# Kernel optimization log

Hardware: AMD Instinct MI355X
Metric: run time of the kernel (lower is better)

The kernel has to match this reference:

```python
import jax, jax.numpy as jnp
import numpy as np

BS = 512          # graphs in batch
G = 5             # n_freq_bands
EL = 32           # electrodes per graph
IN = 5            # in_channels
HC = 64           # first_hc == hidden_channels
N = BS * G * EL   # 81920 nodes
E = N * 16        # 1310720 edges
NC = 3            # n_classes
NUM_LAYERS = 2


def setup_inputs() -> dict:
    key = jax.random.key(0)
    ks = jax.random.split(key, 16)
    s = 0.05
    return {
        "x": jax.random.normal(ks[0], (N, IN), jnp.float32),
        "edge_index": jax.random.randint(ks[1], (2, E), 0, N, dtype=jnp.int32),
        "edge_attr": jax.random.uniform(ks[2], (E,), jnp.float32),
        # GatedGraphConv propagation weights: [num_layers, HC, HC]
        "Wg": jax.random.normal(ks[3], (NUM_LAYERS, HC, HC), jnp.float32) * s,
        # GRUCell params (torch layout: gates r,z,n stacked)
        "w_ih": jax.random.normal(ks[4], (3 * HC, HC), jnp.float32) * s,
        "w_hh": jax.random.normal(ks[5], (3 * HC, HC), jnp.float32) * s,
        "b_ih": jnp.zeros((3 * HC,), jnp.float32),
        "b_hh": jnp.zeros((3 * HC,), jnp.float32),
        # MLP head (torch Linear layout: [out, in])
        "W1": jax.random.normal(ks[6], (HC, G * EL * HC), jnp.float32) * s,
        "b1": jnp.zeros((HC,), jnp.float32),
        "W2": jax.random.normal(ks[7], (HC // 2, HC), jnp.float32) * s,
        "b2": jnp.zeros((HC // 2,), jnp.float32),
        "W3": jax.random.normal(ks[8], (HC // 4, HC // 2), jnp.float32) * s,
        "b3": jnp.zeros((HC // 4,), jnp.float32),
        "W4": jax.random.normal(ks[9], (NC, HC // 4), jnp.float32) * s,
        "b4": jnp.zeros((NC,), jnp.float32),
    }


def _gru_cell(m, h, w_ih, w_hh, b_ih, b_hh):
    gi = m @ w_ih.T + b_ih
    gh = h @ w_hh.T + b_hh
    i_r, i_z, i_n = jnp.split(gi, 3, axis=-1)
    h_r, h_z, h_n = jnp.split(gh, 3, axis=-1)
    r = jax.nn.sigmoid(i_r + h_r)
    z = jax.nn.sigmoid(i_z + h_z)
    n = jnp.tanh(i_n + r * h_n)
    return (1.0 - z) * n + z * h


def reference(x, edge_index, edge_attr, Wg, w_ih, w_hh, b_ih, b_hh,
              W1, b1, W2, b2, W3, b3, W4, b4):
    # GatedGraphConv: zero-pad input features to HC
    h = jnp.pad(x, ((0, 0), (0, HC - IN)))  # [N, HC]
    src, dst = edge_index[0], edge_index[1]
    for i in range(NUM_LAYERS):
        m = h @ Wg[i]                               # [N, HC]
        msg = m[src] * edge_attr[:, None]           # [E, HC] gather + weight
        aggr = jax.ops.segment_sum(msg, dst, num_segments=N)  # scatter-add
        h = _gru_cell(aggr, h, w_ih, w_hh, b_ih, b_hh)
    # rearrange '(bs g e) f -> bs (e g f)'
    h = h.reshape(BS, G, EL, HC).transpose(0, 2, 1, 3).reshape(BS, EL * G * HC)
    z = jax.nn.relu(h @ W1.T + b1)
    z = jax.nn.relu(z @ W2.T + b2)
    z = jax.nn.relu(z @ W3.T + b3)
    logits = z @ W4.T + b4
    return jax.nn.softmax(logits, axis=-1)
```

## Files before the change

kernel.cpp:

```cpp
#include <hip/hip_runtime.h>
#include <cstdint>

#define BSZ 512
#define NG 5
#define NEL 32
#define IN_C 5
#define HC 64
#define NN (BSZ * NG * NEL)
#define NE (NN * 16)
#define NC 3
#define KTOT (NG * NEL * HC)
#define NSLICE 16
#define NCB 160
#define CCHUNK (NE / NCB)
#define SORTCAP 9728

typedef __attribute__((ext_vector_type(8))) short bf16x8;
typedef __attribute__((ext_vector_type(4))) float f32x4;

__device__ __forceinline__ float bcast(float v, int l) {
  return __int_as_float(__builtin_amdgcn_readlane(__float_as_int(v), l));
}

__device__ __forceinline__ ushort bf16r(float f) {
  unsigned u = __float_as_uint(f);
  return (ushort)((u + 0x7FFFu + ((u >> 16) & 1u)) >> 16);
}

__device__ __forceinline__ float bf16f(ushort s) {
  return __uint_as_float(((unsigned)s) << 16);
}

__device__ __forceinline__ bf16x8 packf4(float4 x, float4 y) {
  bf16x8 r;
  r[0] = (short)bf16r(x.x); r[1] = (short)bf16r(x.y);
  r[2] = (short)bf16r(x.z); r[3] = (short)bf16r(x.w);
  r[4] = (short)bf16r(y.x); r[5] = (short)bf16r(y.y);
  r[6] = (short)bf16r(y.z); r[7] = (short)bf16r(y.w);
  return r;
}

__device__ __forceinline__ float sigmoidf_(float x) {
  return 1.0f / (1.0f + __expf(-x));
}

__device__ __forceinline__ float tanhf_(float x) {
  x = fminf(fmaxf(x, -15.0f), 15.0f);
  float e = __expf(2.0f * x);
  return (e - 1.0f) / (e + 1.0f);
}

__global__ void k_init(const float* __restrict__ x, float* __restrict__ h) {
  int idx = blockIdx.x * 256 + threadIdx.x;
  int n = idx >> 6, c = idx & 63;
  h[idx] = (c < IN_C) ? x[n * IN_C + c] : 0.0f;
}

__global__ void __launch_bounds__(256) k_chist(const int* __restrict__ ei,
                                               int* __restrict__ ghist) {
  __shared__ int lh[NCB];
  const int t = threadIdx.x;
  if (t < NCB) lh[t] = 0;
  __syncthreads();
  const int base = blockIdx.x * CCHUNK;
  for (int k = t; k < CCHUNK; k += 256)
    atomicAdd(&lh[ei[NE + base + k] >> 9], 1);
  __syncthreads();
  if (t < NCB) ghist[t * NCB + blockIdx.x] = lh[t];
}

__global__ void k_cscan(const int* __restrict__ ghist, int* __restrict__ cstart,
                        int* __restrict__ gof) {
  __shared__ int tot[NCB];
  __shared__ int cs[NCB + 1];
  const int t = threadIdx.x;
  if (t < NCB) {
    int s = 0;
    const int* g = ghist + t * NCB;
    for (int blk = 0; blk < NCB; ++blk) s += g[blk];
    tot[t] = s;
  }
  __syncthreads();
  if (t == 0) {
    int run = 0;
    for (int i = 0; i < NCB; ++i) { cs[i] = run; run += tot[i]; }
    cs[NCB] = run;
  }
  __syncthreads();
  if (t < NCB + 1) cstart[t] = cs[t];
  if (t < NCB) {
    int run = cs[t];
    const int* g = ghist + t * NCB;
    int* go = gof + t * NCB;
    for (int blk = 0; blk < NCB; ++blk) { go[blk] = run; run += g[blk]; }
  }
}

__global__ void __launch_bounds__(256) k_cpart(const int* __restrict__ ei,
                                               const float* __restrict__ ea,
                                               const int* __restrict__ gof,
                                               int* __restrict__ ent4,
                                               ushort* __restrict__ dstlo) {
  __shared__ int cur[NCB];
  const int t = threadIdx.x;
  if (t < NCB) cur[t] = gof[t * NCB + blockIdx.x];
  __syncthreads();
  const int base = blockIdx.x * CCHUNK;
  for (int k = t; k < CCHUNK; k += 256) {
    int e = base + k;
    int src = ei[e];
    int dst = ei[NE + e];
    ushort bw = bf16r(ea[e]);
    int slot = atomicAdd(&cur[dst >> 9], 1);
    ent4[slot] = src | ((int)bw << 17);
    dstlo[slot] = (ushort)(dst & 511);
  }
}

__global__ void __launch_bounds__(256) k_sort(const int* __restrict__ ent4,
                                              const ushort* __restrict__ dstlo,
                                              const int* __restrict__ cstart,
                                              int* __restrict__ csr4,
                                              int* __restrict__ off,
                                              int* __restrict__ cnt) {
  __shared__ int nh[512];
  __shared__ int part[256];
  __shared__ int sent[SORTCAP];
  const int t = threadIdx.x;
  const int b = blockIdx.x;
  const int r0 = cstart[b];
  const int r1 = cstart[b + 1];
  int len = r1 - r0;
  if (len > SORTCAP) len = SORTCAP;
  nh[t] = 0;
  nh[t + 256] = 0;
  __syncthreads();
  for (int k = t; k < len; k += 256) atomicAdd(&nh[dstlo[r0 + k]], 1);
  __syncthreads();
  int a0 = nh[2 * t], a1 = nh[2 * t + 1];
  part[t] = a0 + a1;
  __syncthreads();
  for (int d = 1; d < 256; d <<= 1) {
    int x = (t >= d) ? part[t - d] : 0;
    __syncthreads();
    part[t] += x;
    __syncthreads();
  }
  const int base = part[t] - a0 - a1;
  const int n0 = b * 512;
  off[n0 + 2 * t] = r0 + base;
  off[n0 + 2 * t + 1] = r0 + base + a0;
  cnt[n0 + 2 * t] = a0;
  cnt[n0 + 2 * t + 1] = a1;
  nh[2 * t] = base;
  nh[2 * t + 1] = base + a0;
  __syncthreads();
  for (int k = t; k < len; k += 256) {
    int d = dstlo[r0 + k];
    int slot = atomicAdd(&nh[d], 1);
    sent[slot] = ent4[r0 + k];
  }
  __syncthreads();
  for (int k = t; k < len; k += 256) csr4[r0 + k] = sent[k];
}


__global__ void __launch_bounds__(256) k_gemm_mfma(
    const float* __restrict__ h, const float* __restrict__ Wg,
    ushort* __restrict__ m16) {
  const int lane = threadIdx.x & 63;
  const int cl = lane & 15;
  const int quad = lane >> 4;
  bf16x8 B[4][2];
#pragma unroll
  for (int ct = 0; ct < 4; ++ct)
#pragma unroll
    for (int kh = 0; kh < 2; ++kh) {
      bf16x8 b;
#pragma unroll
      for (int j = 0; j < 8; ++j)
        b[j] = (short)bf16r(Wg[(kh * 32 + quad * 8 + j) * 64 + ct * 16 + cl]);
      B[ct][kh] = b;
    }
  int g = (blockIdx.x * 256 + threadIdx.x) >> 6;
  const int nwaves = (gridDim.x * 256) >> 6;
  for (; g < NN / 16; g += nwaves) {
    const float* hp = h + (size_t)(g * 16 + cl) * 64 + quad * 8;
    bf16x8 a0 = packf4(*(const float4*)hp, *(const float4*)(hp + 4));
    bf16x8 a1 = packf4(*(const float4*)(hp + 32), *(const float4*)(hp + 36));
    ushort* mp = m16 + (size_t)(g * 16 + quad * 4) * 64 + cl;
#pragma unroll
    for (int ct = 0; ct < 4; ++ct) {
      f32x4 acc = {0.0f, 0.0f, 0.0f, 0.0f};
      acc = __builtin_amdgcn_mfma_f32_16x16x32_bf16(a0, B[ct][0], acc, 0, 0, 0);
      acc = __builtin_amdgcn_mfma_f32_16x16x32_bf16(a1, B[ct][1], acc, 0, 0, 0);
#pragma unroll
      for (int rg = 0; rg < 4; ++rg)
        mp[(size_t)rg * 64 + ct * 16] = bf16r(acc[rg]);
    }
  }
}

__global__ void k_aggregate(const int* __restrict__ off, const int* __restrict__ cnt,
                            const int* __restrict__ csr4, const ushort* __restrict__ m16,
                            ushort* __restrict__ aggr16) {
  const int lane = threadIdx.x & 63;
  int wv = (blockIdx.x * 256 + threadIdx.x) >> 6;
  const int nw = (gridDim.x * 256) >> 6;
  for (int n = wv; n < NN; n += nw) {
    const int r0 = __builtin_amdgcn_readfirstlane(off[n]);
    const int c = __builtin_amdgcn_readfirstlane(cnt[n]);
    int ed = 0;
    if (lane < c) ed = csr4[r0 + lane];
    const int cc = c > 64 ? 64 : c;
    float acc = 0.0f;
    int i = 0;
    for (; i + 8 <= cc; i += 8) {
      int x0 = __builtin_amdgcn_readlane(ed, i + 0);
      int x1 = __builtin_amdgcn_readlane(ed, i + 1);
      int x2 = __builtin_amdgcn_readlane(ed, i + 2);
      int x3 = __builtin_amdgcn_readlane(ed, i + 3);
      int x4 = __builtin_amdgcn_readlane(ed, i + 4);
      int x5 = __builtin_amdgcn_readlane(ed, i + 5);
      int x6 = __builtin_amdgcn_readlane(ed, i + 6);
      int x7 = __builtin_amdgcn_readlane(ed, i + 7);
      float m0 = bf16f(m16[(size_t)(x0 & 0x1FFFF) * 64 + lane]);
      float m1 = bf16f(m16[(size_t)(x1 & 0x1FFFF) * 64 + lane]);
      float m2 = bf16f(m16[(size_t)(x2 & 0x1FFFF) * 64 + lane]);
      float m3 = bf16f(m16[(size_t)(x3 & 0x1FFFF) * 64 + lane]);
      float m4 = bf16f(m16[(size_t)(x4 & 0x1FFFF) * 64 + lane]);
      float m5 = bf16f(m16[(size_t)(x5 & 0x1FFFF) * 64 + lane]);
      float m6 = bf16f(m16[(size_t)(x6 & 0x1FFFF) * 64 + lane]);
      float m7 = bf16f(m16[(size_t)(x7 & 0x1FFFF) * 64 + lane]);
      acc = fmaf(m0, bf16f((ushort)((unsigned)x0 >> 17)), acc);
      acc = fmaf(m1, bf16f((ushort)((unsigned)x1 >> 17)), acc);
      acc = fmaf(m2, bf16f((ushort)((unsigned)x2 >> 17)), acc);
      acc = fmaf(m3, bf16f((ushort)((unsigned)x3 >> 17)), acc);
      acc = fmaf(m4, bf16f((ushort)((unsigned)x4 >> 17)), acc);
      acc = fmaf(m5, bf16f((ushort)((unsigned)x5 >> 17)), acc);
      acc = fmaf(m6, bf16f((ushort)((unsigned)x6 >> 17)), acc);
      acc = fmaf(m7, bf16f((ushort)((unsigned)x7 >> 17)), acc);
    }
    for (; i < cc; ++i) {
      int x = __builtin_amdgcn_readlane(ed, i);
      acc = fmaf(bf16f(m16[(size_t)(x & 0x1FFFF) * 64 + lane]),
                 bf16f((ushort)((unsigned)x >> 17)), acc);
    }
    for (int j = 64; j < c; ++j) {
      int x = csr4[r0 + j];
      acc = fmaf(bf16f(m16[(size_t)(x & 0x1FFFF) * 64 + lane]),
                 bf16f((ushort)((unsigned)x >> 17)), acc);
    }
    aggr16[(size_t)n * 64 + lane] = bf16r(acc);
  }
}

__global__ void __launch_bounds__(256) k_gru_mfma(
    const ushort* __restrict__ aggr16, float* __restrict__ h,
    const float* __restrict__ wih, const float* __restrict__ whh,
    const float* __restrict__ bih, const float* __restrict__ bhh) {
  const int lane = threadIdx.x & 63;
  const int w = threadIdx.x >> 6;
  const int cl = lane & 15;
  const int quad = lane >> 4;
  const int c = w * 16 + cl;

  bf16x8 BI[3][2], BH[3][2];
#pragma unroll
  for (int g3 = 0; g3 < 3; ++g3) {
    const float* wi = wih + (size_t)(g3 * 64 + c) * 64;
    const float* wh = whh + (size_t)(g3 * 64 + c) * 64;
#pragma unroll
    for (int kh = 0; kh < 2; ++kh) {
      const float* p = wi + kh * 32 + quad * 8;
      BI[g3][kh] = packf4(*(const float4*)p, *(const float4*)(p + 4));
      const float* q = wh + kh * 32 + quad * 8;
      BH[g3][kh] = packf4(*(const float4*)q, *(const float4*)(q + 4));
    }
  }
  const float br = bih[c] + bhh[c];
  const float bz = bih[64 + c] + bhh[64 + c];
  const float bni = bih[128 + c];
  const float bnh = bhh[128 + c];

  const int ngroups = NN / 16;
  for (int g = blockIdx.x; g < ngroups; g += gridDim.x) {
    const size_t arow = (size_t)(g * 16 + cl) * 64 + quad * 8;
    bf16x8 a0 = *(const bf16x8*)(aggr16 + arow);
    bf16x8 a1 = *(const bf16x8*)(aggr16 + arow + 32);
    const float* hp = h + arow;
    bf16x8 h0 = packf4(*(const float4*)hp, *(const float4*)(hp + 4));
    bf16x8 h1 = packf4(*(const float4*)(hp + 32), *(const float4*)(hp + 36));
    float hv[4];
    const size_t obase = (size_t)(g * 16 + quad * 4) * 64 + c;
#pragma unroll
    for (int rg = 0; rg < 4; ++rg) hv[rg] = h[obase + (size_t)rg * 64];
    __syncthreads();

    f32x4 zero = {0.0f, 0.0f, 0.0f, 0.0f};
    f32x4 aR = zero, aZ = zero, aN = zero, hR = zero, hZ = zero, hN = zero;
    aR = __builtin_amdgcn_mfma_f32_16x16x32_bf16(a0, BI[0][0], aR, 0, 0, 0);
    aR = __builtin_amdgcn_mfma_f32_16x16x32_bf16(a1, BI[0][1], aR, 0, 0, 0);
    aZ = __builtin_amdgcn_mfma_f32_16x16x32_bf16(a0, BI[1][0], aZ, 0, 0, 0);
    aZ = __builtin_amdgcn_mfma_f32_16x16x32_bf16(a1, BI[1][1], aZ, 0, 0, 0);
    aN = __builtin_amdgcn_mfma_f32_16x16x32_bf16(a0, BI[2][0], aN, 0, 0, 0);
    aN = __builtin_amdgcn_mfma_f32_16x16x32_bf16(a1, BI[2][1], aN, 0, 0, 0);
    hR = __builtin_amdgcn_mfma_f32_16x16x32_bf16(h0, BH[0][0], hR, 0, 0, 0);
    hR = __builtin_amdgcn_mfma_f32_16x16x32_bf16(h1, BH[0][1], hR, 0, 0, 0);
    hZ = __builtin_amdgcn_mfma_f32_16x16x32_bf16(h0, BH[1][0], hZ, 0, 0, 0);
    hZ = __builtin_amdgcn_mfma_f32_16x16x32_bf16(h1, BH[1][1], hZ, 0, 0, 0);
    hN = __builtin_amdgcn_mfma_f32_16x16x32_bf16(h0, BH[2][0], hN, 0, 0, 0);
    hN = __builtin_amdgcn_mfma_f32_16x16x32_bf16(h1, BH[2][1], hN, 0, 0, 0);

#pragma unroll
    for (int rg = 0; rg < 4; ++rg) {
      float r = sigmoidf_(aR[rg] + hR[rg] + br);
      float z = sigmoidf_(aZ[rg] + hZ[rg] + bz);
      float nv = tanhf_(aN[rg] + bni + r * (hN[rg] + bnh));
      h[obase + (size_t)rg * 64] = (1.0f - z) * nv + z * hv[rg];
    }
  }
}

__global__ void __launch_bounds__(256) k_mlp1_mfma(
    const float* __restrict__ h, const float* __restrict__ W1,
    float* __restrict__ part) {
  const int lane = threadIdx.x & 63;
  const int w = threadIdx.x >> 6;
  const int cl = lane & 15;
  const int quad = lane >> 4;
  const int bg = blockIdx.x >> 4;
  const int sl = blockIdx.x & 15;
  const int bs0 = bg * 16;
  const int c = w * 16 + cl;
  f32x4 acc = {0.0f, 0.0f, 0.0f, 0.0f};
#pragma unroll
  for (int e2 = 0; e2 < 2; ++e2) {
    const int e = sl * 2 + e2;
#pragma unroll
    for (int g = 0; g < 5; ++g) {
      const float* hp = h + ((size_t)(bs0 + cl) * 160 + g * 32 + e) * 64 + quad * 8;
      bf16x8 a0 = packf4(*(const float4*)hp, *(const float4*)(hp + 4));
      bf16x8 a1 = packf4(*(const float4*)(hp + 32), *(const float4*)(hp + 36));
      const int kbase = e * 320 + g * 64;
      const float* wp = W1 + (size_t)c * KTOT + kbase + quad * 8;
      bf16x8 b0 = packf4(*(const float4*)wp, *(const float4*)(wp + 4));
      bf16x8 b1 = packf4(*(const float4*)(wp + 32), *(const float4*)(wp + 36));
      acc = __builtin_amdgcn_mfma_f32_16x16x32_bf16(a0, b0, acc, 0, 0, 0);
      acc = __builtin_amdgcn_mfma_f32_16x16x32_bf16(a1, b1, acc, 0, 0, 0);
    }
  }
  float* pp = part + ((size_t)sl * BSZ + bs0 + quad * 4) * 64 + c;
#pragma unroll
  for (int rg = 0; rg < 4; ++rg) pp[(size_t)rg * 64] = acc[rg];
}

__global__ void k_tail(const float* __restrict__ part, const float* __restrict__ b1,
                       const float* __restrict__ W2, const float* __restrict__ b2,
                       const float* __restrict__ W3, const float* __restrict__ b3,
                       const float* __restrict__ W4, const float* __restrict__ b4,
                       float* __restrict__ out) {
  const int lane = threadIdx.x & 63;
  const int bs = blockIdx.x * 4 + (threadIdx.x >> 6);
  float zp = 0.0f;
#pragma unroll
  for (int s = 0; s < NSLICE; ++s) zp += part[((size_t)s * BSZ + bs) * 64 + lane];
  float zv = fmaxf(zp + b1[lane], 0.0f);
  const int c2 = lane & 31;
  float acc2 = b2[c2];
#pragma unroll
  for (int k = 0; k < 64; ++k) acc2 = fmaf(bcast(zv, k), W2[c2 * 64 + k], acc2);
  acc2 = fmaxf(acc2, 0.0f);
  const int c3 = lane & 15;
  float acc3 = b3[c3];
#pragma unroll
  for (int k = 0; k < 32; ++k) acc3 = fmaf(bcast(acc2, k), W3[c3 * 32 + k], acc3);
  acc3 = fmaxf(acc3, 0.0f);
  float l0 = b4[0], l1 = b4[1], l2 = b4[2];
#pragma unroll
  for (int k = 0; k < 16; ++k) {
    float v = bcast(acc3, k);
    l0 = fmaf(v, W4[k], l0);
    l1 = fmaf(v, W4[16 + k], l1);
    l2 = fmaf(v, W4[32 + k], l2);
  }
  float mx = fmaxf(l0, fmaxf(l1, l2));
  float e0 = __expf(l0 - mx), e1 = __expf(l1 - mx), e2 = __expf(l2 - mx);
  float inv = 1.0f / (e0 + e1 + e2);
  if (lane == 0) {
    out[bs * 3 + 0] = e0 * inv;
    out[bs * 3 + 1] = e1 * inv;
    out[bs * 3 + 2] = e2 * inv;
  }
}

extern "C" void kernel_launch(void* const* d_in, const int* in_sizes, int n_in,
                              void* d_out, int out_size, void* d_ws, size_t ws_size,
                              hipStream_t stream) {
  const float* x = (const float*)d_in[0];
  const int* ei = (const int*)d_in[1];
  const float* ea = (const float*)d_in[2];
  const float* Wg = (const float*)d_in[3];
  const float* wih = (const float*)d_in[4];
  const float* whh = (const float*)d_in[5];
  const float* bih = (const float*)d_in[6];
  const float* bhh = (const float*)d_in[7];
  const float* W1 = (const float*)d_in[8];
  const float* b1 = (const float*)d_in[9];
  const float* W2 = (const float*)d_in[10];
  const float* b2 = (const float*)d_in[11];
  const float* W3 = (const float*)d_in[12];
  const float* b3 = (const float*)d_in[13];
  const float* W4 = (const float*)d_in[14];
  const float* b4 = (const float*)d_in[15];
  float* out = (float*)d_out;

  float* h = (float*)d_ws;
  float* part = h + (size_t)NN * 64;
  int* ghist = (int*)(part + (size_t)NSLICE * BSZ * 64);
  int* gof = ghist + NCB * NCB;
  int* cstart = gof + NCB * NCB;
  int* off = cstart + 164;
  int* cnt = off + NN;
  int* ent4 = cnt + NN;
  int* csr4 = ent4 + NE;
  ushort* m16 = (ushort*)(csr4 + NE);
  ushort* aggr16 = m16 + (size_t)NN * 64;
  ushort* dstlo = aggr16 + (size_t)NN * 64;

  k_chist<<<NCB, 256, 0, stream>>>(ei, ghist);
  k_cscan<<<1, 256, 0, stream>>>(ghist, cstart, gof);
  k_cpart<<<NCB, 256, 0, stream>>>(ei, ea, gof, ent4, dstlo);
  k_sort<<<NCB, 256, 0, stream>>>(ent4, dstlo, cstart, csr4, off, cnt);

  k_init<<<NN * 64 / 256, 256, 0, stream>>>(x, h);
  for (int layer = 0; layer < 2; ++layer) {
    k_gemm_mfma<<<1280, 256, 0, stream>>>(h, Wg + layer * 64 * 64, m16);
    k_aggregate<<<2048, 256, 0, stream>>>(off, cnt, csr4, m16, aggr16);
    k_gru_mfma<<<1280, 256, 0, stream>>>(aggr16, h, wih, whh, bih, bhh);
  }
  k_mlp1_mfma<<<512, 256, 0, stream>>>(h, W1, part);
  k_tail<<<BSZ / 4, 256, 0, stream>>>(part, b1, W2, b2, W3, b3, W4, b4, out);
}
```

Before: 367.4 us.

## Store hidden state and W1 in bf16 and refine edge buckets to 256 nodes

Hidden state h is now kept in bf16 throughout, so the GEMM, GRU and MLP1 kernels load packed bf16 directly instead of converting fp32 each time. W1 is converted to bf16 once per call in a new kernel. The coarse edge-partition bucket count doubles to 320 (256 nodes per bucket) with byte-sized dst-low indices and a smaller sort capacity, giving more sort blocks and less shared memory. This cuts memory traffic and conversion work, at the cost of storing h with bf16 rounding between layers, an extra W1 conversion pass, and a tighter SORTCAP that could silently truncate heavy buckets.

```diff
diff --git a/kernel.cpp b/kernel.cpp
--- a/kernel.cpp
+++ b/kernel.cpp
@@ -11,9 +11,9 @@
 #define NC 3
 #define KTOT (NG * NEL * HC)
 #define NSLICE 16
-#define NCB 160
+#define NCB 320
 #define CCHUNK (NE / NCB)
-#define SORTCAP 9728
+#define SORTCAP 5120
 
 typedef __attribute__((ext_vector_type(8))) short bf16x8;
 typedef __attribute__((ext_vector_type(4))) float f32x4;
@@ -29,15 +29,6 @@
 
 __device__ __forceinline__ float bf16f(ushort s) {
   return __uint_as_float(((unsigned)s) << 16);
-}
-
-__device__ __forceinline__ bf16x8 packf4(float4 x, float4 y) {
-  bf16x8 r;
-  r[0] = (short)bf16r(x.x); r[1] = (short)bf16r(x.y);
-  r[2] = (short)bf16r(x.z); r[3] = (short)bf16r(x.w);
-  r[4] = (short)bf16r(y.x); r[5] = (short)bf16r(y.y);
-  r[6] = (short)bf16r(y.z); r[7] = (short)bf16r(y.w);
-  return r;
 }
 
 __device__ __forceinline__ float sigmoidf_(float x) {
@@ -50,23 +41,28 @@
   return (e - 1.0f) / (e + 1.0f);
 }
 
-__global__ void k_init(const float* __restrict__ x, float* __restrict__ h) {
+__global__ void k_init(const float* __restrict__ x, ushort* __restrict__ hb) {
   int idx = blockIdx.x * 256 + threadIdx.x;
   int n = idx >> 6, c = idx & 63;
-  h[idx] = (c < IN_C) ? x[n * IN_C + c] : 0.0f;
+  hb[idx] = (c < IN_C) ? bf16r(x[n * IN_C + c]) : (ushort)0;
+}
+
+__global__ void k_cvtw(const float* __restrict__ W1, ushort* __restrict__ w1b) {
+  int i = blockIdx.x * 256 + threadIdx.x;
+  w1b[i] = bf16r(W1[i]);
 }
 
 __global__ void __launch_bounds__(256) k_chist(const int* __restrict__ ei,
                                                int* __restrict__ ghist) {
   __shared__ int lh[NCB];
   const int t = threadIdx.x;
-  if (t < NCB) lh[t] = 0;
+  for (int i = t; i < NCB; i += 256) lh[i] = 0;
   __syncthreads();
   const int base = blockIdx.x * CCHUNK;
   for (int k = t; k < CCHUNK; k += 256)
-    atomicAdd(&lh[ei[NE + base + k] >> 9], 1);
-  __syncthreads();
-  if (t < NCB) ghist[t * NCB + blockIdx.x] = lh[t];
+    atomicAdd(&lh[ei[NE + base + k] >> 8], 1);
+  __syncthreads();
+  for (int i = t; i < NCB; i += 256) ghist[i * NCB + blockIdx.x] = lh[i];
 }
 
 __global__ void k_cscan(const int* __restrict__ ghist, int* __restrict__ cstart,
@@ -100,10 +96,10 @@
                                                const float* __restrict__ ea,
                                                const int* __restrict__ gof,
                                                int* __restrict__ ent4,
-                                               ushort* __restrict__ dstlo) {
+                                               uchar1* __restrict__ dstlo) {
   __shared__ int cur[NCB];
   const int t = threadIdx.x;
-  if (t < NCB) cur[t] = gof[t * NCB + blockIdx.x];
+  for (int i = t; i < NCB; i += 256) cur[i] = gof[i * NCB + blockIdx.x];
   __syncthreads();
   const int base = blockIdx.x * CCHUNK;
   for (int k = t; k < CCHUNK; k += 256) {
@@ -111,19 +107,19 @@
     int src = ei[e];
     int dst = ei[NE + e];
     ushort bw = bf16r(ea[e]);
-    int slot = atomicAdd(&cur[dst >> 9], 1);
+    int slot = atomicAdd(&cur[dst >> 8], 1);
     ent4[slot] = src | ((int)bw << 17);
-    dstlo[slot] = (ushort)(dst & 511);
+    dstlo[slot].x = (unsigned char)(dst & 255);
   }
 }
 
 __global__ void __launch_bounds__(256) k_sort(const int* __restrict__ ent4,
-                                              const ushort* __restrict__ dstlo,
+                                              const uchar1* __restrict__ dstlo,
                                               const int* __restrict__ cstart,
                                               int* __restrict__ csr4,
                                               int* __restrict__ off,
                                               int* __restrict__ cnt) {
-  __shared__ int nh[512];
+  __shared__ int nh[256];
   __shared__ int part[256];
   __shared__ int sent[SORTCAP];
   const int t = threadIdx.x;
@@ -133,12 +129,11 @@
   int len = r1 - r0;
   if (len > SORTCAP) len = SORTCAP;
   nh[t] = 0;
-  nh[t + 256] = 0;
-  __syncthreads();
-  for (int k = t; k < len; k += 256) atomicAdd(&nh[dstlo[r0 + k]], 1);
-  __syncthreads();
-  int a0 = nh[2 * t], a1 = nh[2 * t + 1];
-  part[t] = a0 + a1;
+  __syncthreads();
+  for (int k = t; k < len; k += 256) atomicAdd(&nh[dstlo[r0 + k].x], 1);
+  __syncthreads();
+  int a0 = nh[t];
+  part[t] = a0;
   __syncthreads();
   for (int d = 1; d < 256; d <<= 1) {
     int x = (t >= d) ? part[t - d] : 0;
@@ -146,17 +141,14 @@
     part[t] += x;
     __syncthreads();
   }
-  const int base = part[t] - a0 - a1;
-  const int n0 = b * 512;
-  off[n0 + 2 * t] = r0 + base;
-  off[n0 + 2 * t + 1] = r0 + base + a0;
-  cnt[n0 + 2 * t] = a0;
-  cnt[n0 + 2 * t + 1] = a1;
-  nh[2 * t] = base;
-  nh[2 * t + 1] = base + a0;
+  const int base = part[t] - a0;
+  const int n0 = b * 256;
+  off[n0 + t] = r0 + base;
+  cnt[n0 + t] = a0;
+  nh[t] = base;
   __syncthreads();
   for (int k = t; k < len; k += 256) {
-    int d = dstlo[r0 + k];
+    int d = dstlo[r0 + k].x;
     int slot = atomicAdd(&nh[d], 1);
     sent[slot] = ent4[r0 + k];
   }
@@ -166,7 +158,7 @@
 
 
 __global__ void __launch_bounds__(256) k_gemm_mfma(
-    const float* __restrict__ h, const float* __restrict__ Wg,
+    const ushort* __restrict__ hb, const float* __restrict__ Wg,
     ushort* __restrict__ m16) {
   const int lane = threadIdx.x & 63;
   const int cl = lane & 15;
@@ -185,9 +177,9 @@
   int g = (blockIdx.x * 256 + threadIdx.x) >> 6;
   const int nwaves = (gridDim.x * 256) >> 6;
   for (; g < NN / 16; g += nwaves) {
-    const float* hp = h + (size_t)(g * 16 + cl) * 64 + quad * 8;
-    bf16x8 a0 = packf4(*(const float4*)hp, *(const float4*)(hp + 4));
-    bf16x8 a1 = packf4(*(const float4*)(hp + 32), *(const float4*)(hp + 36));
+    const ushort* hp = hb + (size_t)(g * 16 + cl) * 64 + quad * 8;
+    bf16x8 a0 = *(const bf16x8*)hp;
+    bf16x8 a1 = *(const bf16x8*)(hp + 32);
     ushort* mp = m16 + (size_t)(g * 16 + quad * 4) * 64 + cl;
 #pragma unroll
     for (int ct = 0; ct < 4; ++ct) {
@@ -256,7 +248,7 @@
 }
 
 __global__ void __launch_bounds__(256) k_gru_mfma(
-    const ushort* __restrict__ aggr16, float* __restrict__ h,
+    const ushort* __restrict__ aggr16, ushort* __restrict__ hb,
     const float* __restrict__ wih, const float* __restrict__ whh,
     const float* __restrict__ bih, const float* __restrict__ bhh) {
   const int lane = threadIdx.x & 63;
@@ -272,10 +264,14 @@
     const float* wh = whh + (size_t)(g3 * 64 + c) * 64;
 #pragma unroll
     for (int kh = 0; kh < 2; ++kh) {
-      const float* p = wi + kh * 32 + quad * 8;
-      BI[g3][kh] = packf4(*(const float4*)p, *(const float4*)(p + 4));
-      const float* q = wh + kh * 32 + quad * 8;
-      BH[g3][kh] = packf4(*(const float4*)q, *(const float4*)(q + 4));
+      bf16x8 bi, bh;
+#pragma unroll
+      for (int j = 0; j < 8; ++j) {
+        bi[j] = (short)bf16r(wi[kh * 32 + quad * 8 + j]);
+        bh[j] = (short)bf16r(wh[kh * 32 + quad * 8 + j]);
+      }
+      BI[g3][kh] = bi;
+      BH[g3][kh] = bh;
     }
   }
   const float br = bih[c] + bhh[c];
@@ -288,13 +284,12 @@
     const size_t arow = (size_t)(g * 16 + cl) * 64 + quad * 8;
     bf16x8 a0 = *(const bf16x8*)(aggr16 + arow);
     bf16x8 a1 = *(const bf16x8*)(aggr16 + arow + 32);
-    const float* hp = h + arow;
-    bf16x8 h0 = packf4(*(const float4*)hp, *(const float4*)(hp + 4));
-    bf16x8 h1 = packf4(*(const float4*)(hp + 32), *(const float4*)(hp + 36));
+    bf16x8 h0 = *(const bf16x8*)(hb + arow);
+    bf16x8 h1 = *(const bf16x8*)(hb + arow + 32);
     float hv[4];
     const size_t obase = (size_t)(g * 16 + quad * 4) * 64 + c;
 #pragma unroll
-    for (int rg = 0; rg < 4; ++rg) hv[rg] = h[obase + (size_t)rg * 64];
+    for (int rg = 0; rg < 4; ++rg) hv[rg] = bf16f(hb[obase + (size_t)rg * 64]);
     __syncthreads();
 
     f32x4 zero = {0.0f, 0.0f, 0.0f, 0.0f};
@@ -317,13 +312,13 @@
       float r = sigmoidf_(aR[rg] + hR[rg] + br);
       float z = sigmoidf_(aZ[rg] + hZ[rg] + bz);
       float nv = tanhf_(aN[rg] + bni + r * (hN[rg] + bnh));
-      h[obase + (size_t)rg * 64] = (1.0f - z) * nv + z * hv[rg];
+      hb[obase + (size_t)rg * 64] = bf16r((1.0f - z) * nv + z * hv[rg]);
     }
   }
 }
 
 __global__ void __launch_bounds__(256) k_mlp1_mfma(
-    const float* __restrict__ h, const float* __restrict__ W1,
+    const ushort* __restrict__ hb, const ushort* __restrict__ w1b,
     float* __restrict__ part) {
   const int lane = threadIdx.x & 63;
   const int w = threadIdx.x >> 6;
@@ -339,13 +334,13 @@
     const int e = sl * 2 + e2;
 #pragma unroll
     for (int g = 0; g < 5; ++g) {
-      const float* hp = h + ((size_t)(bs0 + cl) * 160 + g * 32 + e) * 64 + quad * 8;
-      bf16x8 a0 = packf4(*(const float4*)hp, *(const float4*)(hp + 4));
-      bf16x8 a1 = packf4(*(const float4*)(hp + 32), *(const float4*)(hp + 36));
+      const ushort* hp = hb + ((size_t)(bs0 + cl) * 160 + g * 32 + e) * 64 + quad * 8;
+      bf16x8 a0 = *(const bf16x8*)hp;
+      bf16x8 a1 = *(const bf16x8*)(hp + 32);
       const int kbase = e * 320 + g * 64;
-      const float* wp = W1 + (size_t)c * KTOT + kbase + quad * 8;
-      bf16x8 b0 = packf4(*(const float4*)wp, *(const float4*)(wp + 4));
-      bf16x8 b1 = packf4(*(const float4*)(wp + 32), *(const float4*)(wp + 36));
+      const ushort* wp = w1b + (size_t)c * KTOT + kbase + quad * 8;
+      bf16x8 b0 = *(const bf16x8*)wp;
+      bf16x8 b1 = *(const bf16x8*)(wp + 32);
       acc = __builtin_amdgcn_mfma_f32_16x16x32_bf16(a0, b0, acc, 0, 0, 0);
       acc = __builtin_amdgcn_mfma_f32_16x16x32_bf16(a1, b1, acc, 0, 0, 0);
     }
@@ -415,30 +410,32 @@
   const float* b4 = (const float*)d_in[15];
   float* out = (float*)d_out;
 
-  float* h = (float*)d_ws;
-  float* part = h + (size_t)NN * 64;
+  float* part = (float*)d_ws;
   int* ghist = (int*)(part + (size_t)NSLICE * BSZ * 64);
   int* gof = ghist + NCB * NCB;
   int* cstart = gof + NCB * NCB;
-  int* off = cstart + 164;
+  int* off = cstart + 324;
   int* cnt = off + NN;
   int* ent4 = cnt + NN;
   int* csr4 = ent4 + NE;
-  ushort* m16 = (ushort*)(csr4 + NE);
+  ushort* hb = (ushort*)(csr4 + NE);
+  ushort* m16 = hb + (size_t)NN * 64;
   ushort* aggr16 = m16 + (size_t)NN * 64;
-  ushort* dstlo = aggr16 + (size_t)NN * 64;
+  ushort* w1b = aggr16 + (size_t)NN * 64;
+  uchar1* dstlo = (uchar1*)(w1b + (size_t)KTOT * HC);
 
   k_chist<<<NCB, 256, 0, stream>>>(ei, ghist);
-  k_cscan<<<1, 256, 0, stream>>>(ghist, cstart, gof);
+  k_cscan<<<1, 320, 0, stream>>>(ghist, cstart, gof);
   k_cpart<<<NCB, 256, 0, stream>>>(ei, ea, gof, ent4, dstlo);
   k_sort<<<NCB, 256, 0, stream>>>(ent4, dstlo, cstart, csr4, off, cnt);
-
-  k_init<<<NN * 64 / 256, 256, 0, stream>>>(x, h);
+  k_cvtw<<<KTOT * HC / 256, 256, 0, stream>>>(W1, w1b);
+
+  k_init<<<NN * 64 / 256, 256, 0, stream>>>(x, hb);
   for (int layer = 0; layer < 2; ++layer) {
-    k_gemm_mfma<<<1280, 256, 0, stream>>>(h, Wg + layer * 64 * 64, m16);
+    k_gemm_mfma<<<1280, 256, 0, stream>>>(hb, Wg + layer * 64 * 64, m16);
     k_aggregate<<<2048, 256, 0, stream>>>(off, cnt, csr4, m16, aggr16);
-    k_gru_mfma<<<1280, 256, 0, stream>>>(aggr16, h, wih, whh, bih, bhh);
-  }
-  k_mlp1_mfma<<<512, 256, 0, stream>>>(h, W1, part);
+    k_gru_mfma<<<1280, 256, 0, stream>>>(aggr16, hb, wih, whh, bih, bhh);
+  }
+  k_mlp1_mfma<<<512, 256, 0, stream>>>(hb, w1b, part);
   k_tail<<<BSZ / 4, 256, 0, stream>>>(part, b1, W2, b2, W3, b3, W4, b4, out);
 }
```

Result: slower. 374.7 us (+2.0%).
